# Optimization experiments

Measured on AMD Instinct MI355X. Metric: run time of the kernel, lower is better.

Reference implementation:

```python
import jax, jax.numpy as jnp
import numpy as np
from jax import lax

KS = 3       # kernel_size
PAD = 1      # padding
STRIDE = 1
DIL = 2      # dilation (scales adaptive offsets)
N = KS * KS
DN = ('NCHW', 'OIHW', 'NCHW')


def _conv(x, w, stride, padding):
    return lax.conv_general_dilated(x, w, (stride, stride),
                                    [(padding, padding), (padding, padding)],
                                    dimension_numbers=DN)


def _deform_forward(x, w_p, b_p, w_m, w_ad, w_conv):
    B, C, H, W = x.shape
    offset = _conv(x, w_p, STRIDE, 1) + b_p[None, :, None, None]      # (B,2N,H,W)
    ad_base = 1.0 - jax.nn.sigmoid(_conv(x, w_ad, STRIDE, 1))         # (B,KS,H,W)
    ad = jnp.tile(ad_base, (1, 2 * KS, 1, 1)) * DIL                   # (B,2N,H,W)
    ad_m = jnp.tile((ad_base - 0.5) * 2.0, (1, KS, 1, 1)) * DIL       # (B,N,H,W)
    m = jax.nn.sigmoid(_conv(x, w_m, STRIDE, 1))                      # (B,N,H,W)

    # kernel relative offsets p_n: (1,2N,1,1)
    r = jnp.arange(-(KS - 1) // 2, (KS - 1) // 2 + 1, dtype=x.dtype)
    pnx, pny = jnp.meshgrid(r, r, indexing='ij')
    p_n = jnp.concatenate([pnx.ravel(), pny.ravel()])[None, :, None, None]
    # base sampling coords p_0: (1,2N,H,W), offset by 1 to match zero padding
    ix = jnp.arange(1, H * STRIDE + 1, STRIDE, dtype=x.dtype)
    iy = jnp.arange(1, W * STRIDE + 1, STRIDE, dtype=x.dtype)
    p0x, p0y = jnp.meshgrid(ix, iy, indexing='ij')
    p_0 = jnp.concatenate([jnp.broadcast_to(p0x, (1, N, H, W)),
                           jnp.broadcast_to(p0y, (1, N, H, W))], axis=1)

    p = p_0 + p_n + offset + ad * p_n                                  # (B,2N,H,W)
    p = p.transpose(0, 2, 3, 1)                                        # (B,H,W,2N)

    xp = jnp.pad(x, ((0, 0), (0, 0), (PAD, PAD), (PAD, PAD)))         # (B,C,Hp,Wp)
    Hp, Wp = H + 2 * PAD, W + 2 * PAD

    q_lt = jnp.floor(p)
    q_rb = q_lt + 1.0

    def clampxy(q):
        return jnp.concatenate([jnp.clip(q[..., :N], 0, Hp - 1),
                                jnp.clip(q[..., N:], 0, Wp - 1)], -1).astype(jnp.int32)

    q_lt = clampxy(q_lt)
    q_rb = clampxy(q_rb)
    q_lb = jnp.concatenate([q_lt[..., :N], q_rb[..., N:]], -1)
    q_rt = jnp.concatenate([q_rb[..., :N], q_lt[..., N:]], -1)

    # out-of-range mask (detached); snap those points to floor, then clamp
    mask = jnp.concatenate([
        (p[..., :N] < PAD) | (p[..., :N] > Hp - 1 - PAD),
        (p[..., N:] < PAD) | (p[..., N:] > Wp - 1 - PAD)], -1).astype(p.dtype)
    mask = lax.stop_gradient(mask)
    p = p * (1 - mask) + jnp.floor(p) * mask
    p = jnp.concatenate([jnp.clip(p[..., :N], 0, Hp - 1),
                         jnp.clip(p[..., N:], 0, Wp - 1)], -1)

    def g(q, sx, sy):  # bilinear weights
        qx = q[..., :N].astype(p.dtype)
        qy = q[..., N:].astype(p.dtype)
        return (1 + sx * (qx - p[..., :N])) * (1 + sy * (qy - p[..., N:]))

    g_lt = g(q_lt, 1, 1)
    g_rb = g(q_rb, -1, -1)
    g_lb = g(q_lb, 1, -1)
    g_rt = g(q_rt, -1, 1)

    x_flat = xp.reshape(B, C, Hp * Wp)
    L = H * W * N

    def gather(q):
        idx = (q[..., :N] * Wp + q[..., N:]).reshape(B, 1, L)
        idx = jnp.broadcast_to(idx, (B, C, L))
        return jnp.take_along_axis(x_flat, idx, axis=2).reshape(B, C, H, W, N)

    x_off = (g_lt[:, None] * gather(q_lt) + g_rb[:, None] * gather(q_rb)
             + g_lb[:, None] * gather(q_lb) + g_rt[:, None] * gather(q_rt))

    # modulation scaled by adaptive term
    mm = (m * ad_m).transpose(0, 2, 3, 1)[:, None]                     # (B,1,H,W,N)
    x_off = x_off * mm

    # (B,C,H,W,ks*ks) -> (B,C,H*ks,W*ks)
    x_off = x_off.reshape(B, C, H, W, KS, KS).transpose(0, 1, 2, 4, 3, 5)
    x_off = x_off.reshape(B, C, H * KS, W * KS)
    return _conv(x_off, w_conv, KS, 0)                                 # (B,Cout,H,W)


def setup_inputs() -> dict:
    key = jax.random.key(0)
    ks = jax.random.split(key, 6)
    C_in, C_out = 64, 64
    x = jax.random.normal(ks[0], (2, C_in, 128, 128), jnp.float32)
    w_p = jax.random.normal(ks[1], (2 * N, C_in, 3, 3), jnp.float32) * 0.01
    b_p = jax.random.normal(ks[2], (2 * N,), jnp.float32) * 0.01
    w_m = jax.random.normal(ks[3], (N, C_in, 3, 3), jnp.float32) * 0.05
    w_ad = jax.random.normal(ks[4], (KS, C_in, 3, 3), jnp.float32) * 0.05
    w_conv = jax.random.normal(ks[5], (C_out, C_in, KS, KS), jnp.float32) / np.sqrt(C_in * N).astype(np.float32)
    return {"x": x, "w_p": w_p, "b_p": b_p, "w_m": w_m, "w_ad": w_ad, "w_conv": w_conv}


def reference(x, w_p, b_p, w_m, w_ad, w_conv):
    return _deform_forward(x, w_p, b_p, w_m, w_ad, w_conv)
```

## Files before the change

kernel.cpp:

```cpp
#include <hip/hip_runtime.h>
#include <hip/hip_fp16.h>
#include <math.h>

#define H 128
#define W 128
#define BATCH 2

typedef short short8 __attribute__((ext_vector_type(8)));
typedef float f32x4 __attribute__((ext_vector_type(4)));
typedef float f32x16 __attribute__((ext_vector_type(16)));

#define BPLANE 1081600
#define PLANE  2163200
#define XS_M   PLANE
#define WC_OFF (2 * PLANE)
#define WM_OFF (WC_OFF + 36864)
#define WM_PLANE 18432
#define META_OFF (WM_OFF + 2 * WM_PLANE)

__device__ __forceinline__ unsigned f2bf_u(float f) {
    union { float f; unsigned u; } v; v.f = f;
    return (v.u + 0x7FFFu + ((v.u >> 16) & 1u)) >> 16;
}
__device__ __forceinline__ float bfbits2f(unsigned lo16) {
    union { unsigned u; float f; } v; v.u = lo16 << 16;
    return v.f;
}
__device__ __forceinline__ float bfs2f(short s) {
    union { unsigned u; float f; } v; v.u = ((unsigned)(unsigned short)s) << 16;
    return v.f;
}
__device__ __forceinline__ void split2(float v, unsigned& h, unsigned& m) {
    h = f2bf_u(v);
    float r1 = v - bfbits2f(h);
    m = f2bf_u(r1);
}

__global__ __launch_bounds__(512) void prep_kernel(
    const float* __restrict__ x, const float* __restrict__ w_p,
    const float* __restrict__ w_m, const float* __restrict__ w_ad,
    const float* __restrict__ w_conv, unsigned short* __restrict__ ws)
{
    const int blk = blockIdx.x, t = threadIdx.x;
    if (blk < 528) {
        int xcd = blk & 7, rest = blk >> 3;
        int chalf = rest & 1, q = rest >> 1;
        int sub = xcd & 3, b = xcd >> 2;
        int hrow;
        if (sub == 0)      { if (q > 32) return; hrow = q; }
        else if (sub == 3) { if (q > 32) return; hrow = 97 + q; }
        else               { if (q > 31) return; hrow = sub * 32 + 1 + q; }
        size_t rb = ((size_t)b * 16900 + hrow * 130) * 32;
        unsigned* uh = (unsigned*)ws + rb;
        unsigned* um = (unsigned*)(ws + XS_M) + rb;
        if (hrow == 0 || hrow == 129) {
            for (int f = t + chalf * 2080; f < 2080 + chalf * 2080; f += 512) {
                uh[f] = 0; um[f] = 0;
            }
            return;
        }
        __shared__ float s[64 * 65];
        int h = hrow - 1;
        for (int f = t; f < 64 * 16; f += 512) {
            int ci = f >> 4, w4 = f & 15;
            *(float4*)&s[ci * 65 + w4 * 4] =
                *(const float4*)&x[((size_t)(b * 64 + ci) * 128 + h) * 128 + chalf * 64 + w4 * 4];
        }
        __syncthreads();
        {
            int f = t;
            int w = f >> 3, g = f & 7;
            unsigned hv[4], mv[4];
            #pragma unroll
            for (int p = 0; p < 4; ++p) {
                int cip = g * 4 + p;
                unsigned h0, m0, h1, m1;
                split2(s[(2 * cip) * 65 + w], h0, m0);
                split2(s[(2 * cip + 1) * 65 + w], h1, m1);
                hv[p] = h0 | (h1 << 16);
                mv[p] = m0 | (m1 << 16);
            }
            int o = (chalf * 64 + w + 1) * 32 + g * 4;
            *(uint4*)&uh[o] = make_uint4(hv[0], hv[1], hv[2], hv[3]);
            *(uint4*)&um[o] = make_uint4(mv[0], mv[1], mv[2], mv[3]);
        }
        if (chalf == 0) { if (t < 32) { uh[t] = 0; um[t] = 0; } }
        else           { if (t < 32) { int o = 129 * 32 + t; uh[o] = 0; um[o] = 0; } }
    } else if (blk < 546) {
        int q = (blk - 528) * 512 + t;
        int e = q * 4;
        int j = e & 15, co = (e >> 4) & 63, kk = e >> 10;
        int klin = kk * 16 + j;
        int n = klin >> 6, ci = klin & 63;
        const float* src = w_conv + co * 576 + n;
        ushort4 r;
        r.x = (unsigned short)f2bf_u(src[(ci + 0) * 9]);
        r.y = (unsigned short)f2bf_u(src[(ci + 1) * 9]);
        r.z = (unsigned short)f2bf_u(src[(ci + 2) * 9]);
        r.w = (unsigned short)f2bf_u(src[(ci + 3) * 9]);
        *(ushort4*)(ws + WC_OFF + e) = r;
    } else {
        int q = (blk - 546) * 512 + t;
        int oc = q / 576, k = q % 576;
        int s = k >> 6, ci = k & 63;
        float v = 0.f;
        if (oc < 18)      v = w_p[oc * 576 + ci * 9 + s];
        else if (oc < 21) v = w_ad[(oc - 18) * 576 + ci * 9 + s];
        else if (oc < 30) v = w_m[(oc - 21) * 576 + ci * 9 + s];
        unsigned hh, mm; split2(v, hh, mm);
        ws[WM_OFF + q] = (unsigned short)hh;
        ws[WM_OFF + WM_PLANE + q] = (unsigned short)mm;
    }
}

__global__ __launch_bounds__(512, 2) void meta_kernel(
    const float* __restrict__ b_p, const unsigned short* __restrict__ wsu,
    float* __restrict__ meta)
{
    __shared__ __align__(16) unsigned short s_w[64 * 584];
    const int t = threadIdx.x;
    const int d = blockIdx.x;
    const int l = (d & 7) * 32 + (d >> 3);
    const int b = l >> 7, i = l & 127;

    const int wv = t >> 6, lane = t & 63, lr = lane & 15, lg = lane >> 4;
    const int px = wv * 16 + lr;
    const unsigned short* xsb = wsu + (size_t)b * BPLANE;

    const unsigned short* bp_pre = xsb + (i * 130 + px) * 64 + lg * 8;
    short8 pre_bh0 = *(const short8*)(bp_pre);
    short8 pre_bm0 = *(const short8*)(bp_pre + XS_M);
    short8 pre_bh1 = *(const short8*)(bp_pre + 32);
    short8 pre_bm1 = *(const short8*)(bp_pre + 32 + XS_M);

    #pragma unroll
    for (int it = 0; it < 9; ++it) {
        int chunk = it * 512 + t;
        int r = chunk / 72, c8 = chunk % 72;
        *(short8*)(s_w + r * 584 + c8 * 8) =
            *(const short8*)(wsu + WM_OFF + chunk * 8);
    }
    __syncthreads();

    f32x4 aA0 = {0,0,0,0}, aB0 = {0,0,0,0}, aA1 = {0,0,0,0}, aB1 = {0,0,0,0};
    #pragma unroll
    for (int kk = 0; kk < 18; ++kk) {
        const int s = kk >> 1;
        short8 bh, bm;
        if (kk == 0)      { bh = pre_bh0; bm = pre_bm0; }
        else if (kk == 1) { bh = pre_bh1; bm = pre_bm1; }
        else {
            const unsigned short* bp = xsb + ((i + s / 3) * 130 + (px + s % 3)) * 64
                                       + ((kk & 1) << 5) + lg * 8;
            bh = *(const short8*)(bp);
            bm = *(const short8*)(bp + XS_M);
        }
        const unsigned short* w0 = s_w + lr * 584 + kk * 32 + lg * 8;
        short8 ah0 = *(const short8*)(w0);
        short8 am0 = *(const short8*)(w0 + 32 * 584);
        const unsigned short* w1 = w0 + 16 * 584;
        short8 ah1 = *(const short8*)(w1);
        short8 am1 = *(const short8*)(w1 + 32 * 584);
        aA0 = __builtin_amdgcn_mfma_f32_16x16x32_bf16(ah0, bh, aA0, 0, 0, 0);
        aB0 = __builtin_amdgcn_mfma_f32_16x16x32_bf16(ah0, bm, aB0, 0, 0, 0);
        aA0 = __builtin_amdgcn_mfma_f32_16x16x32_bf16(am0, bh, aA0, 0, 0, 0);
        aA1 = __builtin_amdgcn_mfma_f32_16x16x32_bf16(ah1, bh, aA1, 0, 0, 0);
        aB1 = __builtin_amdgcn_mfma_f32_16x16x32_bf16(ah1, bm, aB1, 0, 0, 0);
        aA1 = __builtin_amdgcn_mfma_f32_16x16x32_bf16(am1, bh, aA1, 0, 0, 0);
    }

    float* mb = meta + (((size_t)b * 128 + i) * 128 + px) * 32;
    {
        const float4 bq = *(const float4*)(b_p + lg * 4);
        f32x4 o0;
        o0[0] = aA0[0] + aB0[0] + bq.x;
        o0[1] = aA0[1] + aB0[1] + bq.y;
        o0[2] = aA0[2] + aB0[2] + bq.z;
        o0[3] = aA0[3] + aB0[3] + bq.w;
        *(f32x4*)(mb + lg * 4) = o0;
    }
    {
        f32x4 o1;
        #pragma unroll
        for (int r = 0; r < 4; ++r) {
            int oc = 16 + lg * 4 + r;
            float v = aA1[r] + aB1[r];
            if (oc < 18)      v += b_p[oc];
            else if (oc < 21) v = 1.f - 1.f / (1.f + expf(-v));
            else              v = 1.f / (1.f + expf(-v));
            o1[r] = v;
        }
        *(f32x4*)(mb + 16 + lg * 4) = o1;
    }
}

__global__ __launch_bounds__(512, 8) void deform_kernel(
    const unsigned short* __restrict__ wsu, const float* __restrict__ meta,
    float* __restrict__ out)
{
    __shared__ __align__(16) char smem[40832];
    unsigned short* s_valb = (unsigned short*)smem;
    __half2* s_gh = (__half2*)(smem + 37376);
    int* s_idxp = (int*)(smem + 39680);

    const int t = threadIdx.x;
    const int d = blockIdx.x;
    const int l = (d & 7) * 128 + (d >> 3);
    const int jb = l & 3, i = (l >> 2) & 127, b = l >> 9;
    const int j0 = jb * 32;

    if (t < 288) {
        int pix = t / 9, n = t % 9;
        int ki = n / 3, kj = n % 3;
        const float* mrow = meta + (((size_t)b * 128 + i) * 128 + j0 + pix) * 32;
        float adb  = mrow[18 + kj];
        float offx = mrow[n];
        float offy = mrow[9 + n];
        float msig = mrow[21 + n];
        float pnx = (float)(ki - 1), pny = (float)(kj - 1);
        float pxc = (float)(i + 1)        + pnx + offx + 2.f * adb * pnx;
        float pyc = (float)(j0 + pix + 1) + pny + offy + 2.f * adb * pny;

        float flx = floorf(pxc), fly = floorf(pyc);
        int ix0 = (int)fminf(fmaxf(flx,       0.f), 129.f);
        int ix1 = (int)fminf(fmaxf(flx + 1.f, 0.f), 129.f);
        int iy0 = (int)fminf(fmaxf(fly,       0.f), 129.f);
        int iy1 = (int)fminf(fmaxf(fly + 1.f, 0.f), 129.f);

        float ptx = (pxc < 1.f || pxc > 128.f) ? flx : pxc;
        float pty = (pyc < 1.f || pyc > 128.f) ? fly : pyc;
        ptx = fminf(fmaxf(ptx, 0.f), 129.f);
        pty = fminf(fmaxf(pty, 0.f), 129.f);

        float wxl = 1.f + (float)ix0 - ptx;
        float wxr = 1.f - ((float)ix1 - ptx);
        float wyl = 1.f + (float)iy0 - pty;
        float wyr = 1.f - ((float)iy1 - pty);

        float mm = msig * (adb - 0.5f) * 4.f;

        s_gh[t * 2 + 0] = __floats2half2_rn(wxl * wyl * mm, wxr * wyr * mm);
        s_gh[t * 2 + 1] = __floats2half2_rn(wxl * wyr * mm, wxr * wyl * mm);
        s_idxp[t] = ix0 | (ix1 << 8) | (iy0 << 16) | (iy1 << 24);
    }
    __syncthreads();

    const unsigned short* xsb = wsu + (size_t)b * BPLANE;
    #define GATHER(TASK) do {                                                     \
        int task = (TASK);                                                        \
        int n = task >> 8, pix = (task >> 3) & 31, cig = task & 7;                \
        int pk = s_idxp[pix * 9 + n];                                             \
        int ix0 = pk & 255, ix1 = (pk >> 8) & 255;                                \
        int iy0 = (pk >> 16) & 255, iy1 = (pk >> 24) & 255;                       \
        const unsigned short* base = xsb + cig * 8;                               \
        short8 v00 = *(const short8*)(base + (ix0 * 130 + iy0) * 64);             \
        short8 v11 = *(const short8*)(base + (ix1 * 130 + iy1) * 64);             \
        short8 v01 = *(const short8*)(base + (ix0 * 130 + iy1) * 64);             \
        short8 v10 = *(const short8*)(base + (ix1 * 130 + iy0) * 64);             \
        float2 g01 = __half22float2(s_gh[(pix * 9 + n) * 2 + 0]);                 \
        float2 g23 = __half22float2(s_gh[(pix * 9 + n) * 2 + 1]);                 \
        unsigned po[4];                                                           \
        _Pragma("unroll")                                                         \
        for (int jp = 0; jp < 4; ++jp) {                                          \
            float e0 = g01.x * bfs2f(v00[2 * jp])     + g01.y * bfs2f(v11[2 * jp])\
                     + g23.x * bfs2f(v01[2 * jp])     + g23.y * bfs2f(v10[2 * jp]);\
            float e1 = g01.x * bfs2f(v00[2 * jp + 1]) + g01.y * bfs2f(v11[2 * jp + 1])\
                     + g23.x * bfs2f(v01[2 * jp + 1]) + g23.y * bfs2f(v10[2 * jp + 1]);\
            po[jp] = f2bf_u(e0) | (f2bf_u(e1) << 16);                             \
        }                                                                         \
        *(uint4*)(s_valb + pix * 584 + n * 64 + cig * 8)                          \
            = make_uint4(po[0], po[1], po[2], po[3]);                             \
    } while (0)

    #pragma unroll
    for (int it = 0; it < 4; ++it) GATHER(t + it * 512);
    if (t < 256) GATHER(t + 2048);
    #undef GATHER
    __syncthreads();

    {
        const int w = t >> 6, lane = t & 63;
        const int ch = w & 1, kq = w >> 1;
        const int colA = lane & 31, hi = lane >> 5;
        const unsigned short* wa = wsu + WC_OFF + ((kq * 9) * 64 + ch * 32 + colA) * 16 + hi * 8;
        const unsigned short* vb = s_valb + colA * 584 + (kq * 9) * 16 + hi * 8;
        f32x16 acc = {0,0,0,0,0,0,0,0,0,0,0,0,0,0,0,0};
        #pragma unroll
        for (int s = 0; s < 9; ++s) {
            short8 a   = *(const short8*)(wa + s * 1024);
            short8 bfr = *(const short8*)(vb + s * 16);
            acc = __builtin_amdgcn_mfma_f32_32x32x16_bf16(a, bfr, acc, 0, 0, 0);
        }
        __syncthreads();
        float* sp = (float*)smem;
        #pragma unroll
        for (int r = 0; r < 16; ++r)
            sp[(w * 16 + r) * 65 + lane] = acc[r];
        __syncthreads();
        int ch2 = t >> 8, e = t & 255;
        int lane2 = e & 63, rq = e >> 6;
        #pragma unroll
        for (int q = 0; q < 4; ++q) {
            int reg = rq * 4 + q;
            float v = sp[((0 + ch2) * 16 + reg) * 65 + lane2]
                    + sp[((2 + ch2) * 16 + reg) * 65 + lane2]
                    + sp[((4 + ch2) * 16 + reg) * 65 + lane2]
                    + sp[((6 + ch2) * 16 + reg) * 65 + lane2];
            int col = lane2 & 31;
            int row = (reg & 3) + 8 * (reg >> 2) + 4 * (lane2 >> 5);
            int co = ch2 * 32 + row;
            out[(((size_t)b * 64 + co) * 128 + i) * 128 + j0 + col] = v;
        }
    }
}

extern "C" void kernel_launch(void* const* d_in, const int* in_sizes, int n_in,
                              void* d_out, int out_size, void* d_ws, size_t ws_size,
                              hipStream_t stream) {
    const float* x      = (const float*)d_in[0];
    const float* w_p    = (const float*)d_in[1];
    const float* b_p    = (const float*)d_in[2];
    const float* w_m    = (const float*)d_in[3];
    const float* w_ad   = (const float*)d_in[4];
    const float* w_conv = (const float*)d_in[5];
    float* outp = (float*)d_out;
    unsigned short* ws = (unsigned short*)d_ws;
    float* meta_f = (float*)(ws + META_OFF);

    prep_kernel<<<582, 512, 0, stream>>>(x, w_p, w_m, w_ad, w_conv, ws);
    meta_kernel<<<256, 512, 0, stream>>>(b_p, ws, meta_f);
    deform_kernel<<<1024, 512, 0, stream>>>(ws, meta_f, outp);
}
```

Before: 34.25 us.

## Fuse meta conv and deformable gather/conv into one kernel per row

Merges the offset/mask convolution kernel and the deformable sampling plus output convolution kernel into one kernel. Each block computes the metadata for a full image row into shared memory, then loops over four 32-pixel column chunks to gather and convolve. This removes the global metadata round trip and one launch. In exchange the grid shrinks from 1024 deform blocks to 256 blocks with more shared memory each, and the chunks within a block run serially, which lowers parallelism and occupancy.

```diff
diff --git a/kernel.cpp b/kernel.cpp
--- a/kernel.cpp
+++ b/kernel.cpp
@@ -16,7 +16,6 @@
 #define WC_OFF (2 * PLANE)
 #define WM_OFF (WC_OFF + 36864)
 #define WM_PLANE 18432
-#define META_OFF (WM_OFF + 2 * WM_PLANE)
 
 __device__ __forceinline__ unsigned f2bf_u(float f) {
     union { float f; unsigned u; } v; v.f = f;
@@ -113,25 +112,24 @@
     }
 }
 
-__global__ __launch_bounds__(512, 2) void meta_kernel(
+__global__ __launch_bounds__(512, 4) void meta_deform_kernel(
     const float* __restrict__ b_p, const unsigned short* __restrict__ wsu,
-    float* __restrict__ meta)
+    float* __restrict__ out)
 {
-    __shared__ __align__(16) unsigned short s_w[64 * 584];
+    __shared__ __align__(16) char smem[74752];
+    unsigned short* s_w = (unsigned short*)smem;
+    float* s_meta = (float*)(smem + 37376);
+    unsigned short* s_valb = (unsigned short*)smem;
+    __half2* s_gh = (__half2*)(smem + 53760);
+    int* s_idxp = (int*)(smem + 56064);
+
     const int t = threadIdx.x;
     const int d = blockIdx.x;
     const int l = (d & 7) * 32 + (d >> 3);
     const int b = l >> 7, i = l & 127;
+    const unsigned short* xsb = wsu + (size_t)b * BPLANE;
 
     const int wv = t >> 6, lane = t & 63, lr = lane & 15, lg = lane >> 4;
-    const int px = wv * 16 + lr;
-    const unsigned short* xsb = wsu + (size_t)b * BPLANE;
-
-    const unsigned short* bp_pre = xsb + (i * 130 + px) * 64 + lg * 8;
-    short8 pre_bh0 = *(const short8*)(bp_pre);
-    short8 pre_bm0 = *(const short8*)(bp_pre + XS_M);
-    short8 pre_bh1 = *(const short8*)(bp_pre + 32);
-    short8 pre_bm1 = *(const short8*)(bp_pre + 32 + XS_M);
 
     #pragma unroll
     for (int it = 0; it < 9; ++it) {
@@ -141,176 +139,162 @@
             *(const short8*)(wsu + WM_OFF + chunk * 8);
     }
     __syncthreads();
-
-    f32x4 aA0 = {0,0,0,0}, aB0 = {0,0,0,0}, aA1 = {0,0,0,0}, aB1 = {0,0,0,0};
-    #pragma unroll
-    for (int kk = 0; kk < 18; ++kk) {
-        const int s = kk >> 1;
-        short8 bh, bm;
-        if (kk == 0)      { bh = pre_bh0; bm = pre_bm0; }
-        else if (kk == 1) { bh = pre_bh1; bm = pre_bm1; }
-        else {
+    {
+        const int px = wv * 16 + lr;
+        f32x4 aA0 = {0,0,0,0}, aB0 = {0,0,0,0}, aA1 = {0,0,0,0}, aB1 = {0,0,0,0};
+        #pragma unroll
+        for (int kk = 0; kk < 18; ++kk) {
+            const int s = kk >> 1;
             const unsigned short* bp = xsb + ((i + s / 3) * 130 + (px + s % 3)) * 64
                                        + ((kk & 1) << 5) + lg * 8;
-            bh = *(const short8*)(bp);
-            bm = *(const short8*)(bp + XS_M);
-        }
-        const unsigned short* w0 = s_w + lr * 584 + kk * 32 + lg * 8;
-        short8 ah0 = *(const short8*)(w0);
-        short8 am0 = *(const short8*)(w0 + 32 * 584);
-        const unsigned short* w1 = w0 + 16 * 584;
-        short8 ah1 = *(const short8*)(w1);
-        short8 am1 = *(const short8*)(w1 + 32 * 584);
-        aA0 = __builtin_amdgcn_mfma_f32_16x16x32_bf16(ah0, bh, aA0, 0, 0, 0);
-        aB0 = __builtin_amdgcn_mfma_f32_16x16x32_bf16(ah0, bm, aB0, 0, 0, 0);
-        aA0 = __builtin_amdgcn_mfma_f32_16x16x32_bf16(am0, bh, aA0, 0, 0, 0);
-        aA1 = __builtin_amdgcn_mfma_f32_16x16x32_bf16(ah1, bh, aA1, 0, 0, 0);
-        aB1 = __builtin_amdgcn_mfma_f32_16x16x32_bf16(ah1, bm, aB1, 0, 0, 0);
-        aA1 = __builtin_amdgcn_mfma_f32_16x16x32_bf16(am1, bh, aA1, 0, 0, 0);
-    }
-
-    float* mb = meta + (((size_t)b * 128 + i) * 128 + px) * 32;
-    {
-        const float4 bq = *(const float4*)(b_p + lg * 4);
-        f32x4 o0;
-        o0[0] = aA0[0] + aB0[0] + bq.x;
-        o0[1] = aA0[1] + aB0[1] + bq.y;
-        o0[2] = aA0[2] + aB0[2] + bq.z;
-        o0[3] = aA0[3] + aB0[3] + bq.w;
-        *(f32x4*)(mb + lg * 4) = o0;
-    }
-    {
-        f32x4 o1;
-        #pragma unroll
-        for (int r = 0; r < 4; ++r) {
-            int oc = 16 + lg * 4 + r;
-            float v = aA1[r] + aB1[r];
-            if (oc < 18)      v += b_p[oc];
-            else if (oc < 21) v = 1.f - 1.f / (1.f + expf(-v));
-            else              v = 1.f / (1.f + expf(-v));
-            o1[r] = v;
-        }
-        *(f32x4*)(mb + 16 + lg * 4) = o1;
-    }
-}
-
-__global__ __launch_bounds__(512, 8) void deform_kernel(
-    const unsigned short* __restrict__ wsu, const float* __restrict__ meta,
-    float* __restrict__ out)
-{
-    __shared__ __align__(16) char smem[40832];
-    unsigned short* s_valb = (unsigned short*)smem;
-    __half2* s_gh = (__half2*)(smem + 37376);
-    int* s_idxp = (int*)(smem + 39680);
-
-    const int t = threadIdx.x;
-    const int d = blockIdx.x;
-    const int l = (d & 7) * 128 + (d >> 3);
-    const int jb = l & 3, i = (l >> 2) & 127, b = l >> 9;
-    const int j0 = jb * 32;
-
-    if (t < 288) {
-        int pix = t / 9, n = t % 9;
-        int ki = n / 3, kj = n % 3;
-        const float* mrow = meta + (((size_t)b * 128 + i) * 128 + j0 + pix) * 32;
-        float adb  = mrow[18 + kj];
-        float offx = mrow[n];
-        float offy = mrow[9 + n];
-        float msig = mrow[21 + n];
-        float pnx = (float)(ki - 1), pny = (float)(kj - 1);
-        float pxc = (float)(i + 1)        + pnx + offx + 2.f * adb * pnx;
-        float pyc = (float)(j0 + pix + 1) + pny + offy + 2.f * adb * pny;
-
-        float flx = floorf(pxc), fly = floorf(pyc);
-        int ix0 = (int)fminf(fmaxf(flx,       0.f), 129.f);
-        int ix1 = (int)fminf(fmaxf(flx + 1.f, 0.f), 129.f);
-        int iy0 = (int)fminf(fmaxf(fly,       0.f), 129.f);
-        int iy1 = (int)fminf(fmaxf(fly + 1.f, 0.f), 129.f);
-
-        float ptx = (pxc < 1.f || pxc > 128.f) ? flx : pxc;
-        float pty = (pyc < 1.f || pyc > 128.f) ? fly : pyc;
-        ptx = fminf(fmaxf(ptx, 0.f), 129.f);
-        pty = fminf(fmaxf(pty, 0.f), 129.f);
-
-        float wxl = 1.f + (float)ix0 - ptx;
-        float wxr = 1.f - ((float)ix1 - ptx);
-        float wyl = 1.f + (float)iy0 - pty;
-        float wyr = 1.f - ((float)iy1 - pty);
-
-        float mm = msig * (adb - 0.5f) * 4.f;
-
-        s_gh[t * 2 + 0] = __floats2half2_rn(wxl * wyl * mm, wxr * wyr * mm);
-        s_gh[t * 2 + 1] = __floats2half2_rn(wxl * wyr * mm, wxr * wyl * mm);
-        s_idxp[t] = ix0 | (ix1 << 8) | (iy0 << 16) | (iy1 << 24);
+            short8 bh = *(const short8*)(bp);
+            short8 bm = *(const short8*)(bp + XS_M);
+            const unsigned short* w0 = s_w + lr * 584 + kk * 32 + lg * 8;
+            short8 ah0 = *(const short8*)(w0);
+            short8 am0 = *(const short8*)(w0 + 32 * 584);
+            const unsigned short* w1 = w0 + 16 * 584;
+            short8 ah1 = *(const short8*)(w1);
+            short8 am1 = *(const short8*)(w1 + 32 * 584);
+            aA0 = __builtin_amdgcn_mfma_f32_16x16x32_bf16(ah0, bh, aA0, 0, 0, 0);
+            aB0 = __builtin_amdgcn_mfma_f32_16x16x32_bf16(ah0, bm, aB0, 0, 0, 0);
+            aA0 = __builtin_amdgcn_mfma_f32_16x16x32_bf16(am0, bh, aA0, 0, 0, 0);
+            aA1 = __builtin_amdgcn_mfma_f32_16x16x32_bf16(ah1, bh, aA1, 0, 0, 0);
+            aB1 = __builtin_amdgcn_mfma_f32_16x16x32_bf16(ah1, bm, aB1, 0, 0, 0);
+            aA1 = __builtin_amdgcn_mfma_f32_16x16x32_bf16(am1, bh, aA1, 0, 0, 0);
+        }
+        __syncthreads();
+        {
+            const float4 bq = *(const float4*)(b_p + lg * 4);
+            f32x4 o0;
+            o0[0] = aA0[0] + aB0[0] + bq.x;
+            o0[1] = aA0[1] + aB0[1] + bq.y;
+            o0[2] = aA0[2] + aB0[2] + bq.z;
+            o0[3] = aA0[3] + aB0[3] + bq.w;
+            *(f32x4*)(s_meta + px * 32 + lg * 4) = o0;
+        }
+        {
+            f32x4 o1;
+            #pragma unroll
+            for (int r = 0; r < 4; ++r) {
+                int oc = 16 + lg * 4 + r;
+                float v = aA1[r] + aB1[r];
+                if (oc < 18)      v += b_p[oc];
+                else if (oc < 21) v = 1.f - 1.f / (1.f + expf(-v));
+                else              v = 1.f / (1.f + expf(-v));
+                o1[r] = v;
+            }
+            *(f32x4*)(s_meta + px * 32 + 16 + lg * 4) = o1;
+        }
     }
     __syncthreads();
 
-    const unsigned short* xsb = wsu + (size_t)b * BPLANE;
-    #define GATHER(TASK) do {                                                     \
-        int task = (TASK);                                                        \
-        int n = task >> 8, pix = (task >> 3) & 31, cig = task & 7;                \
-        int pk = s_idxp[pix * 9 + n];                                             \
-        int ix0 = pk & 255, ix1 = (pk >> 8) & 255;                                \
-        int iy0 = (pk >> 16) & 255, iy1 = (pk >> 24) & 255;                       \
-        const unsigned short* base = xsb + cig * 8;                               \
-        short8 v00 = *(const short8*)(base + (ix0 * 130 + iy0) * 64);             \
-        short8 v11 = *(const short8*)(base + (ix1 * 130 + iy1) * 64);             \
-        short8 v01 = *(const short8*)(base + (ix0 * 130 + iy1) * 64);             \
-        short8 v10 = *(const short8*)(base + (ix1 * 130 + iy0) * 64);             \
-        float2 g01 = __half22float2(s_gh[(pix * 9 + n) * 2 + 0]);                 \
-        float2 g23 = __half22float2(s_gh[(pix * 9 + n) * 2 + 1]);                 \
-        unsigned po[4];                                                           \
-        _Pragma("unroll")                                                         \
-        for (int jp = 0; jp < 4; ++jp) {                                          \
-            float e0 = g01.x * bfs2f(v00[2 * jp])     + g01.y * bfs2f(v11[2 * jp])\
-                     + g23.x * bfs2f(v01[2 * jp])     + g23.y * bfs2f(v10[2 * jp]);\
-            float e1 = g01.x * bfs2f(v00[2 * jp + 1]) + g01.y * bfs2f(v11[2 * jp + 1])\
-                     + g23.x * bfs2f(v01[2 * jp + 1]) + g23.y * bfs2f(v10[2 * jp + 1]);\
-            po[jp] = f2bf_u(e0) | (f2bf_u(e1) << 16);                             \
-        }                                                                         \
-        *(uint4*)(s_valb + pix * 584 + n * 64 + cig * 8)                          \
-            = make_uint4(po[0], po[1], po[2], po[3]);                             \
-    } while (0)
-
-    #pragma unroll
-    for (int it = 0; it < 4; ++it) GATHER(t + it * 512);
-    if (t < 256) GATHER(t + 2048);
-    #undef GATHER
-    __syncthreads();
-
-    {
-        const int w = t >> 6, lane = t & 63;
-        const int ch = w & 1, kq = w >> 1;
-        const int colA = lane & 31, hi = lane >> 5;
-        const unsigned short* wa = wsu + WC_OFF + ((kq * 9) * 64 + ch * 32 + colA) * 16 + hi * 8;
-        const unsigned short* vb = s_valb + colA * 584 + (kq * 9) * 16 + hi * 8;
-        f32x16 acc = {0,0,0,0,0,0,0,0,0,0,0,0,0,0,0,0};
+    for (int jb2 = 0; jb2 < 4; ++jb2) {
+        const int j0 = jb2 * 32;
+
+        if (t < 288) {
+            int pix = t / 9, n = t % 9;
+            int ki = n / 3, kj = n % 3;
+            const float* mrow = s_meta + (j0 + pix) * 32;
+            float adb  = mrow[18 + kj];
+            float offx = mrow[n];
+            float offy = mrow[9 + n];
+            float msig = mrow[21 + n];
+            float pnx = (float)(ki - 1), pny = (float)(kj - 1);
+            float pxc = (float)(i + 1)        + pnx + offx + 2.f * adb * pnx;
+            float pyc = (float)(j0 + pix + 1) + pny + offy + 2.f * adb * pny;
+
+            float flx = floorf(pxc), fly = floorf(pyc);
+            int ix0 = (int)fminf(fmaxf(flx,       0.f), 129.f);
+            int ix1 = (int)fminf(fmaxf(flx + 1.f, 0.f), 129.f);
+            int iy0 = (int)fminf(fmaxf(fly,       0.f), 129.f);
+            int iy1 = (int)fminf(fmaxf(fly + 1.f, 0.f), 129.f);
+
+            float ptx = (pxc < 1.f || pxc > 128.f) ? flx : pxc;
+            float pty = (pyc < 1.f || pyc > 128.f) ? fly : pyc;
+            ptx = fminf(fmaxf(ptx, 0.f), 129.f);
+            pty = fminf(fmaxf(pty, 0.f), 129.f);
+
+            float wxl = 1.f + (float)ix0 - ptx;
+            float wxr = 1.f - ((float)ix1 - ptx);
+            float wyl = 1.f + (float)iy0 - pty;
+            float wyr = 1.f - ((float)iy1 - pty);
+
+            float mm = msig * (adb - 0.5f) * 4.f;
+
+            s_gh[t * 2 + 0] = __floats2half2_rn(wxl * wyl * mm, wxr * wyr * mm);
+            s_gh[t * 2 + 1] = __floats2half2_rn(wxl * wyr * mm, wxr * wyl * mm);
+            s_idxp[t] = ix0 | (ix1 << 8) | (iy0 << 16) | (iy1 << 24);
+        }
+        __syncthreads();
+
+        #define GATHER(TASK) do {                                                     \
+            int task = (TASK);                                                        \
+            int n = task >> 8, pix = (task >> 3) & 31, cig = task & 7;                \
+            int pk = s_idxp[pix * 9 + n];                                             \
+            int ix0 = pk & 255, ix1 = (pk >> 8) & 255;                                \
+            int iy0 = (pk >> 16) & 255, iy1 = (pk >> 24) & 255;                       \
+            const unsigned short* base = xsb + cig * 8;                               \
+            short8 v00 = *(const short8*)(base + (ix0 * 130 + iy0) * 64);             \
+            short8 v11 = *(const short8*)(base + (ix1 * 130 + iy1) * 64);             \
+            short8 v01 = *(const short8*)(base + (ix0 * 130 + iy1) * 64);             \
+            short8 v10 = *(const short8*)(base + (ix1 * 130 + iy0) * 64);             \
+            float2 g01 = __half22float2(s_gh[(pix * 9 + n) * 2 + 0]);                 \
+            float2 g23 = __half22float2(s_gh[(pix * 9 + n) * 2 + 1]);                 \
+            unsigned po[4];                                                           \
+            _Pragma("unroll")                                                         \
+            for (int jp = 0; jp < 4; ++jp) {                                          \
+                float e0 = g01.x * bfs2f(v00[2 * jp])     + g01.y * bfs2f(v11[2 * jp])\
+                         + g23.x * bfs2f(v01[2 * jp])     + g23.y * bfs2f(v10[2 * jp]);\
+                float e1 = g01.x * bfs2f(v00[2 * jp + 1]) + g01.y * bfs2f(v11[2 * jp + 1])\
+                         + g23.x * bfs2f(v01[2 * jp + 1]) + g23.y * bfs2f(v10[2 * jp + 1]);\
+                po[jp] = f2bf_u(e0) | (f2bf_u(e1) << 16);                             \
+            }                                                                         \
+            *(uint4*)(s_valb + pix * 584 + n * 64 + cig * 8)                          \
+                = make_uint4(po[0], po[1], po[2], po[3]);                             \
+        } while (0)
+
         #pragma unroll
-        for (int s = 0; s < 9; ++s) {
-            short8 a   = *(const short8*)(wa + s * 1024);
-            short8 bfr = *(const short8*)(vb + s * 16);
-            acc = __builtin_amdgcn_mfma_f32_32x32x16_bf16(a, bfr, acc, 0, 0, 0);
-        }
-        __syncthreads();
-        float* sp = (float*)smem;
-        #pragma unroll
-        for (int r = 0; r < 16; ++r)
-            sp[(w * 16 + r) * 65 + lane] = acc[r];
-        __syncthreads();
-        int ch2 = t >> 8, e = t & 255;
-        int lane2 = e & 63, rq = e >> 6;
-        #pragma unroll
-        for (int q = 0; q < 4; ++q) {
-            int reg = rq * 4 + q;
-            float v = sp[((0 + ch2) * 16 + reg) * 65 + lane2]
-                    + sp[((2 + ch2) * 16 + reg) * 65 + lane2]
-                    + sp[((4 + ch2) * 16 + reg) * 65 + lane2]
-                    + sp[((6 + ch2) * 16 + reg) * 65 + lane2];
-            int col = lane2 & 31;
-            int row = (reg & 3) + 8 * (reg >> 2) + 4 * (lane2 >> 5);
-            int co = ch2 * 32 + row;
-            out[(((size_t)b * 64 + co) * 128 + i) * 128 + j0 + col] = v;
-        }
+        for (int it = 0; it < 4; ++it) GATHER(t + it * 512);
+        if (t < 256) GATHER(t + 2048);
+        #undef GATHER
+        __syncthreads();
+
+        {
+            const int w = wv;
+            const int ch = w & 1, kq = w >> 1;
+            const int colA = lane & 31, hi = lane >> 5;
+            const unsigned short* wa = wsu + WC_OFF
+                + ((kq * 9) * 64 + ch * 32 + colA) * 16 + hi * 8;
+            const unsigned short* vb = s_valb + colA * 584 + (kq * 9) * 16 + hi * 8;
+            f32x16 acc = {0,0,0,0,0,0,0,0,0,0,0,0,0,0,0,0};
+            #pragma unroll
+            for (int s = 0; s < 9; ++s) {
+                short8 a   = *(const short8*)(wa + s * 1024);
+                short8 bfr = *(const short8*)(vb + s * 16);
+                acc = __builtin_amdgcn_mfma_f32_32x32x16_bf16(a, bfr, acc, 0, 0, 0);
+            }
+            __syncthreads();
+            float* sp = (float*)smem;
+            #pragma unroll
+            for (int r = 0; r < 16; ++r)
+                sp[(w * 16 + r) * 65 + lane] = acc[r];
+            __syncthreads();
+            int ch2 = t >> 8, e = t & 255;
+            int lane2 = e & 63, rq = e >> 6;
+            #pragma unroll
+            for (int q = 0; q < 4; ++q) {
+                int reg = rq * 4 + q;
+                float v = sp[((0 + ch2) * 16 + reg) * 65 + lane2]
+                        + sp[((2 + ch2) * 16 + reg) * 65 + lane2]
+                        + sp[((4 + ch2) * 16 + reg) * 65 + lane2]
+                        + sp[((6 + ch2) * 16 + reg) * 65 + lane2];
+                int col = lane2 & 31;
+                int row = (reg & 3) + 8 * (reg >> 2) + 4 * (lane2 >> 5);
+                int co = ch2 * 32 + row;
+                out[(((size_t)b * 64 + co) * 128 + i) * 128 + j0 + col] = v;
+            }
+        }
+        __syncthreads();
     }
 }
 
@@ -325,9 +309,7 @@
     const float* w_conv = (const float*)d_in[5];
     float* outp = (float*)d_out;
     unsigned short* ws = (unsigned short*)d_ws;
-    float* meta_f = (float*)(ws + META_OFF);
 
     prep_kernel<<<582, 512, 0, stream>>>(x, w_p, w_m, w_ad, w_conv, ws);
-    meta_kernel<<<256, 512, 0, stream>>>(b_p, ws, meta_f);
-    deform_kernel<<<1024, 512, 0, stream>>>(ws, meta_f, outp);
-}
+    meta_deform_kernel<<<256, 512, 0, stream>>>(b_p, ws, outp);
+}
```

Result: slower. 35.90 us (+4.8%).
